# Performance work log

Measured on AMD Instinct MI355X. Metric: run time of the kernel, lower is better.

The kernel has to match this reference:

```python
import jax, jax.numpy as jnp
import numpy as np

SCALE = 100.0

def square_distance(src, dst):
    # src: [B,N,D], dst: [B,M,D] -> [B,N,M] squared euclidean distances
    d = -2.0 * jnp.einsum('bnd,bmd->bnm', src, dst)
    d = d + jnp.sum(src * src, axis=-1)[:, :, None]
    d = d + jnp.sum(dst * dst, axis=-1)[:, None, :]
    return d

def setup_inputs() -> dict:
    key = jax.random.key(0)
    k1, k2 = jax.random.split(key)
    B, N, M, D = 8, 8192, 8192, 3
    pred = jax.random.normal(k1, (B, N, D), dtype=jnp.float32)
    gt = jax.random.normal(k2, (B, M, D), dtype=jnp.float32)
    return {"pred": pred, "gt": gt}

def reference(pred, gt):
    dis = square_distance(pred, gt)              # [B,N,M]
    pred_to_gt = jnp.min(dis, axis=2).mean(axis=1)  # [B]
    gt_to_pred = jnp.min(dis, axis=1).mean(axis=1)  # [B]
    return (0.5 * pred_to_gt + 0.5 * gt_to_pred).mean() * SCALE
```

## Files before the change

kernel.cpp:

```cpp
#include <hip/hip_runtime.h>


#define B_DIM 8
#define N_DIM 8192
#define MT    (N_DIM / 32)
#define CH    16
#define NC    (MT / CH)
#define BLOCK 256
#define PPW   2

typedef short  bf16x8 __attribute__((ext_vector_type(8)));
typedef float  f32x16 __attribute__((ext_vector_type(16)));

__device__ __forceinline__ unsigned short bf16_rne(float f) {
    unsigned int u = __float_as_uint(f);
    u += 0x7fffu + ((u >> 16) & 1u);
    return (unsigned short)(u >> 16);
}
__device__ __forceinline__ float bf16f(unsigned short h) {
    return __uint_as_float(((unsigned int)h) << 16);
}

__global__ __launch_bounds__(256) void chamfer_prep(
    const float* __restrict__ pred, const float* __restrict__ gt,
    unsigned short* __restrict__ bpack, float* __restrict__ out)
{
    const int i   = blockIdx.x * 256 + threadIdx.x;
    if (i == 0) out[0] = 0.0f;
    const int dir = i >> 16;
    const int bm  = i & 0xFFFF;
    const float* dst = dir ? pred : gt;
    const float x = dst[3*bm+0], y = dst[3*bm+1], z = dst[3*bm+2];
    const unsigned short hx = bf16_rne(x), hy = bf16_rne(y), hz = bf16_rne(z);
    const unsigned short lx = bf16_rne(x - bf16f(hx));
    const unsigned short ly = bf16_rne(y - bf16f(hy));
    const unsigned short lz = bf16_rne(z - bf16f(hz));
    const float gn = x*x + y*y + z*z;
    const unsigned short gnh = bf16_rne(gn), gnl = bf16_rne(gn - bf16f(gnh));
    const unsigned short one = 0x3F80;

    const int b  = bm >> 13, m = bm & (N_DIM - 1);
    const int mt = m >> 5,   c = m & 31;
    const int dirb = (dir << 3) | b;
    unsigned short* p0 = bpack + ((size_t)(dirb * MT + mt) * 64 + c) * 8;
    unsigned short* p1 = p0 + 32 * 8;
    bf16x8 h0 = {(short)hx,(short)hy,(short)hz,(short)lx,(short)ly,(short)lz,(short)hx,(short)hy};
    bf16x8 h1 = {(short)hz,(short)one,(short)one,(short)gnh,(short)gnl,0,0,0};
    *(bf16x8*)p0 = h0;
    *(bf16x8*)p1 = h1;
}

__global__ __launch_bounds__(BLOCK, 2) void chamfer_partial(
    const float* __restrict__ pred, const float* __restrict__ gt,
    const bf16x8* __restrict__ bpack, float* __restrict__ out)
{
    __shared__ bf16x8 sbuf[2][CH * 64];
    __shared__ float wsum[4];
    const int dirb = blockIdx.x;
    const int dir  = dirb >> 3, b = dirb & 7;
    const int w    = threadIdx.x >> 6, lane = threadIdx.x & 63;
    const int half = lane >> 5,  col = lane & 31;

    const float* src  = dir ? gt : pred;
    const float* srcb = src + (size_t)b * N_DIM * 3;

    bf16x8 afrag[PPW];
    #pragma unroll
    for (int p = 0; p < PPW; ++p) {
        const int ntile = (blockIdx.y * 4 + w) * PPW + p;
        const int n = ntile * 32 + col;
        const float x = srcb[3*n+0], y = srcb[3*n+1], z = srcb[3*n+2];
        const float ax = -2.f*x, ay = -2.f*y, az = -2.f*z;
        const unsigned short ahx = bf16_rne(ax), ahy = bf16_rne(ay), ahz = bf16_rne(az);
        const unsigned short alx = bf16_rne(ax - bf16f(ahx));
        const unsigned short aly = bf16_rne(ay - bf16f(ahy));
        const unsigned short alz = bf16_rne(az - bf16f(ahz));
        const float pn = x*x + y*y + z*z;
        const unsigned short pnh = bf16_rne(pn), pnl = bf16_rne(pn - bf16f(pnh));
        const unsigned short one = 0x3F80;
        bf16x8 a0 = {(short)ahx,(short)ahy,(short)ahz,(short)ahx,(short)ahy,(short)ahz,(short)alx,(short)aly};
        bf16x8 a1 = {(short)alz,(short)pnh,(short)pnl,(short)one,(short)one,0,0,0};
        afrag[p] = (half == 0) ? a0 : a1;
    }

    const bf16x8* bp = bpack + (size_t)dirb * MT * 64;
    const f32x16 czero = {0.f,0.f,0.f,0.f,0.f,0.f,0.f,0.f,
                          0.f,0.f,0.f,0.f,0.f,0.f,0.f,0.f};
    float best[PPW][16];
    #pragma unroll
    for (int p = 0; p < PPW; ++p)
        #pragma unroll
        for (int r = 0; r < 16; ++r) best[p][r] = 1e30f;

    bf16x8 rg[4];
    const int soff = w * 256 + lane;
    #define GLOAD(c) { const bf16x8* g = bp + (size_t)(c) * (CH*64) + soff; \
        _Pragma("unroll") for (int i = 0; i < 4; ++i) rg[i] = g[i * 64]; }
    #define SWRITE(pb) { bf16x8* s = &sbuf[pb][soff]; \
        _Pragma("unroll") for (int i = 0; i < 4; ++i) s[i * 64] = rg[i]; }

    GLOAD(0); SWRITE(0); GLOAD(1);
    __syncthreads();

    for (int c = 0; c < NC; ++c) {
        const int pb = c & 1;
        if (c + 1 < NC) SWRITE(pb ^ 1);
        if (c + 2 < NC) GLOAD(c + 2);
        #pragma unroll 8
        for (int j = 0; j < CH; ++j) {
            const bf16x8 bc = sbuf[pb][j * 64 + lane];
            #pragma unroll
            for (int p = 0; p < PPW; ++p) {
                f32x16 d = __builtin_amdgcn_mfma_f32_32x32x16_bf16(afrag[p], bc, czero, 0, 0, 0);
                #pragma unroll
                for (int r = 0; r < 16; ++r) best[p][r] = fminf(best[p][r], d[r]);
            }
        }
        __syncthreads();
    }

    float bsum = 0.f;
    #pragma unroll
    for (int p = 0; p < PPW; ++p) {
        float s = 0.f;
        #pragma unroll
        for (int r = 0; r < 16; ++r) {
            float v = best[p][r];
            v = fminf(v, __shfl_xor(v, 1,  64));
            v = fminf(v, __shfl_xor(v, 2,  64));
            v = fminf(v, __shfl_xor(v, 4,  64));
            v = fminf(v, __shfl_xor(v, 8,  64));
            v = fminf(v, __shfl_xor(v, 16, 64));
            s += v;
        }
        bsum += s + __shfl_xor(s, 32, 64);
    }
    if (lane == 0) wsum[w] = bsum;
    __syncthreads();
    if (threadIdx.x == 0) {
        const float scale = 100.0f * 0.5f / ((float)B_DIM * (float)N_DIM);
        atomicAdd(out, (wsum[0] + wsum[1] + wsum[2] + wsum[3]) * scale);
    }
}

extern "C" void kernel_launch(void* const* d_in, const int* in_sizes, int n_in,
                              void* d_out, int out_size, void* d_ws, size_t ws_size,
                              hipStream_t stream) {
    const float* pred = (const float*)d_in[0];
    const float* gt   = (const float*)d_in[1];
    float* out = (float*)d_out;
    unsigned short* bpack = (unsigned short*)d_ws;

    chamfer_prep<<<(2 * B_DIM * N_DIM) / 256, 256, 0, stream>>>(pred, gt, bpack, out);

    dim3 grid(16, N_DIM / (32 * 4 * PPW));
    chamfer_partial<<<grid, BLOCK, 0, stream>>>(pred, gt, (const bf16x8*)bpack, out);
}
```

Before: 95.53 us.

## Split M across wave pairs, use direct global-to-LDS loads, raise occupancy

Each block now covers 128 query points instead of 256. The four waves form two pairs over N-tiles, and the waves in a pair take separate halves of the M range. The partial row minima from those halves are combined through LDS at the end. Global data is staged straight into LDS with global_load_lds instead of going through registers, and the launch bound allows 4 blocks per CU. The aim is more blocks in flight and more overlap of loads with MFMA work. The cost is a second LDS reduction step, and the synchronisation of the async LDS loads may be fragile.

```diff
diff --git a/kernel.cpp b/kernel.cpp
--- a/kernel.cpp
+++ b/kernel.cpp
@@ -4,8 +4,8 @@
 #define B_DIM 8
 #define N_DIM 8192
 #define MT    (N_DIM / 32)
-#define CH    16
-#define NC    (MT / CH)
+#define CH    8
+#define NC    16
 #define BLOCK 256
 #define PPW   2
 
@@ -50,16 +50,18 @@
     *(bf16x8*)p1 = h1;
 }
 
-__global__ __launch_bounds__(BLOCK, 2) void chamfer_partial(
+__global__ __launch_bounds__(BLOCK, 4) void chamfer_partial(
     const float* __restrict__ pred, const float* __restrict__ gt,
     const bf16x8* __restrict__ bpack, float* __restrict__ out)
 {
-    __shared__ bf16x8 sbuf[2][CH * 64];
-    __shared__ float wsum[4];
+    __shared__ bf16x8 sbuf[2][1024];
+    __shared__ float wsum[2];
     const int dirb = blockIdx.x;
     const int dir  = dirb >> 3, b = dirb & 7;
     const int w    = threadIdx.x >> 6, lane = threadIdx.x & 63;
-    const int half = lane >> 5,  col = lane & 31;
+    const int halfk = lane >> 5,  col = lane & 31;
+    const int nsub = w & 1;
+    const int mh   = w >> 1;
 
     const float* src  = dir ? gt : pred;
     const float* srcb = src + (size_t)b * N_DIM * 3;
@@ -67,7 +69,7 @@
     bf16x8 afrag[PPW];
     #pragma unroll
     for (int p = 0; p < PPW; ++p) {
-        const int ntile = (blockIdx.y * 4 + w) * PPW + p;
+        const int ntile = blockIdx.y * 4 + nsub * 2 + p;
         const int n = ntile * 32 + col;
         const float x = srcb[3*n+0], y = srcb[3*n+1], z = srcb[3*n+2];
         const float ax = -2.f*x, ay = -2.f*y, az = -2.f*z;
@@ -80,10 +82,16 @@
         const unsigned short one = 0x3F80;
         bf16x8 a0 = {(short)ahx,(short)ahy,(short)ahz,(short)ahx,(short)ahy,(short)ahz,(short)alx,(short)aly};
         bf16x8 a1 = {(short)alz,(short)pnh,(short)pnl,(short)one,(short)one,0,0,0};
-        afrag[p] = (half == 0) ? a0 : a1;
+        afrag[p] = (halfk == 0) ? a0 : a1;
     }
 
-    const bf16x8* bp = bpack + (size_t)dirb * MT * 64;
+    const bf16x8* bp = bpack + (size_t)dirb * (MT * 64);
+
+#define STAGE(pb_, c_) { _Pragma("unroll") for (int i = 0; i < 4; ++i) { \
+        const bf16x8* g_ = bp + ((i >> 1) * 8192 + (c_) * 512 + (i & 1) * 256 + w * 64 + lane); \
+        __builtin_amdgcn_global_load_lds((__attribute__((address_space(1))) void*)g_, \
+            (__attribute__((address_space(3))) void*)&sbuf[pb_][i * 256 + w * 64], 16, 0, 0); } }
+
     const f32x16 czero = {0.f,0.f,0.f,0.f,0.f,0.f,0.f,0.f,
                           0.f,0.f,0.f,0.f,0.f,0.f,0.f,0.f};
     float best[PPW][16];
@@ -92,54 +100,61 @@
         #pragma unroll
         for (int r = 0; r < 16; ++r) best[p][r] = 1e30f;
 
-    bf16x8 rg[4];
-    const int soff = w * 256 + lane;
-    #define GLOAD(c) { const bf16x8* g = bp + (size_t)(c) * (CH*64) + soff; \
-        _Pragma("unroll") for (int i = 0; i < 4; ++i) rg[i] = g[i * 64]; }
-    #define SWRITE(pb) { bf16x8* s = &sbuf[pb][soff]; \
-        _Pragma("unroll") for (int i = 0; i < 4; ++i) s[i * 64] = rg[i]; }
-
-    GLOAD(0); SWRITE(0); GLOAD(1);
+    STAGE(0, 0);
     __syncthreads();
 
     for (int c = 0; c < NC; ++c) {
         const int pb = c & 1;
-        if (c + 1 < NC) SWRITE(pb ^ 1);
-        if (c + 2 < NC) GLOAD(c + 2);
-        #pragma unroll 8
-        for (int j = 0; j < CH; ++j) {
-            const bf16x8 bc = sbuf[pb][j * 64 + lane];
+        if (c + 1 < NC) STAGE(pb ^ 1, c + 1);
+        const bf16x8* sb = &sbuf[pb][mh * 512];
+        #pragma unroll
+        for (int j = 0; j < CH; j += 2) {
+            const bf16x8 bc0 = sb[j * 64 + lane];
+            const bf16x8 bc1 = sb[(j + 1) * 64 + lane];
             #pragma unroll
             for (int p = 0; p < PPW; ++p) {
-                f32x16 d = __builtin_amdgcn_mfma_f32_32x32x16_bf16(afrag[p], bc, czero, 0, 0, 0);
+                const f32x16 d0 = __builtin_amdgcn_mfma_f32_32x32x16_bf16(afrag[p], bc0, czero, 0, 0, 0);
+                const f32x16 d1 = __builtin_amdgcn_mfma_f32_32x32x16_bf16(afrag[p], bc1, czero, 0, 0, 0);
                 #pragma unroll
-                for (int r = 0; r < 16; ++r) best[p][r] = fminf(best[p][r], d[r]);
+                for (int r = 0; r < 16; ++r)
+                    best[p][r] = fminf(fminf(best[p][r], d0[r]), d1[r]);
             }
         }
         __syncthreads();
     }
 
-    float bsum = 0.f;
-    #pragma unroll
-    for (int p = 0; p < PPW; ++p) {
-        float s = 0.f;
+    float* cbuf = (float*)&sbuf[0][0];
+    if (mh == 1) {
         #pragma unroll
-        for (int r = 0; r < 16; ++r) {
-            float v = best[p][r];
-            v = fminf(v, __shfl_xor(v, 1,  64));
-            v = fminf(v, __shfl_xor(v, 2,  64));
-            v = fminf(v, __shfl_xor(v, 4,  64));
-            v = fminf(v, __shfl_xor(v, 8,  64));
-            v = fminf(v, __shfl_xor(v, 16, 64));
-            s += v;
+        for (int p = 0; p < PPW; ++p)
+            #pragma unroll
+            for (int r = 0; r < 16; ++r)
+                cbuf[(p * 16 + r) * 128 + nsub * 64 + lane] = best[p][r];
+    }
+    __syncthreads();
+    if (mh == 0) {
+        float bsum = 0.f;
+        #pragma unroll
+        for (int p = 0; p < PPW; ++p) {
+            float s = 0.f;
+            #pragma unroll
+            for (int r = 0; r < 16; ++r) {
+                float v = fminf(best[p][r], cbuf[(p * 16 + r) * 128 + nsub * 64 + lane]);
+                v = fminf(v, __shfl_xor(v, 1,  64));
+                v = fminf(v, __shfl_xor(v, 2,  64));
+                v = fminf(v, __shfl_xor(v, 4,  64));
+                v = fminf(v, __shfl_xor(v, 8,  64));
+                v = fminf(v, __shfl_xor(v, 16, 64));
+                s += v;
+            }
+            bsum += s + __shfl_xor(s, 32, 64);
         }
-        bsum += s + __shfl_xor(s, 32, 64);
+        if (lane == 0) wsum[nsub] = bsum;
     }
-    if (lane == 0) wsum[w] = bsum;
     __syncthreads();
     if (threadIdx.x == 0) {
         const float scale = 100.0f * 0.5f / ((float)B_DIM * (float)N_DIM);
-        atomicAdd(out, (wsum[0] + wsum[1] + wsum[2] + wsum[3]) * scale);
+        atomicAdd(out, (wsum[0] + wsum[1]) * scale);
     }
 }
 
@@ -153,6 +168,6 @@
 
     chamfer_prep<<<(2 * B_DIM * N_DIM) / 256, 256, 0, stream>>>(pred, gt, bpack, out);
 
-    dim3 grid(16, N_DIM / (32 * 4 * PPW));
+    dim3 grid(16, N_DIM / 128);
     chamfer_partial<<<grid, BLOCK, 0, stream>>>(pred, gt, (const bf16x8*)bpack, out);
 }
```

Measured after the change: 116.8 us. 22.2% more time.

## Stream B fragments from global into registers with inline-asm MFMA and min3 pipeline

Applied to the files above, without the earlier changes.

Drops the LDS double-buffered staging of the packed B tiles. Each wave now loads B fragments straight from global memory into registers, issued one batch ahead. MFMAs are hand-scheduled in inline asm, four per batch, and alternate between two accumulator sets so the v_min3 reductions of one batch overlap the MFMAs of the next. The final atomicAdd is replaced by per-block partial sums written to workspace plus a small third reduction kernel. This removes LDS traffic and barriers, but it depends on L2/cache hits for the repeated global loads, on manual hazard s_nops, and it adds a kernel launch.

```diff
diff --git a/kernel.cpp b/kernel.cpp
--- a/kernel.cpp
+++ b/kernel.cpp
@@ -4,10 +4,9 @@
 #define B_DIM 8
 #define N_DIM 8192
 #define MT    (N_DIM / 32)
-#define CH    16
-#define NC    (MT / CH)
 #define BLOCK 256
 #define PPW   2
+#define NBLK  512
 
 typedef short  bf16x8 __attribute__((ext_vector_type(8)));
 typedef float  f32x16 __attribute__((ext_vector_type(16)));
@@ -52,14 +51,13 @@
 
 __global__ __launch_bounds__(BLOCK, 2) void chamfer_partial(
     const float* __restrict__ pred, const float* __restrict__ gt,
-    const bf16x8* __restrict__ bpack, float* __restrict__ out)
+    const bf16x8* __restrict__ bpack, float* __restrict__ part)
 {
-    __shared__ bf16x8 sbuf[2][CH * 64];
     __shared__ float wsum[4];
     const int dirb = blockIdx.x;
     const int dir  = dirb >> 3, b = dirb & 7;
     const int w    = threadIdx.x >> 6, lane = threadIdx.x & 63;
-    const int half = lane >> 5,  col = lane & 31;
+    const int halfk = lane >> 5,  col = lane & 31;
 
     const float* src  = dir ? gt : pred;
     const float* srcb = src + (size_t)b * N_DIM * 3;
@@ -67,7 +65,7 @@
     bf16x8 afrag[PPW];
     #pragma unroll
     for (int p = 0; p < PPW; ++p) {
-        const int ntile = (blockIdx.y * 4 + w) * PPW + p;
+        const int ntile = blockIdx.y * 8 + w * 2 + p;
         const int n = ntile * 32 + col;
         const float x = srcb[3*n+0], y = srcb[3*n+1], z = srcb[3*n+2];
         const float ax = -2.f*x, ay = -2.f*y, az = -2.f*z;
@@ -80,44 +78,59 @@
         const unsigned short one = 0x3F80;
         bf16x8 a0 = {(short)ahx,(short)ahy,(short)ahz,(short)ahx,(short)ahy,(short)ahz,(short)alx,(short)aly};
         bf16x8 a1 = {(short)alz,(short)pnh,(short)pnl,(short)one,(short)one,0,0,0};
-        afrag[p] = (half == 0) ? a0 : a1;
+        afrag[p] = (halfk == 0) ? a0 : a1;
     }
 
-    const bf16x8* bp = bpack + (size_t)dirb * MT * 64;
-    const f32x16 czero = {0.f,0.f,0.f,0.f,0.f,0.f,0.f,0.f,
-                          0.f,0.f,0.f,0.f,0.f,0.f,0.f,0.f};
     float best[PPW][16];
     #pragma unroll
     for (int p = 0; p < PPW; ++p)
         #pragma unroll
         for (int r = 0; r < 16; ++r) best[p][r] = 1e30f;
 
-    bf16x8 rg[4];
-    const int soff = w * 256 + lane;
-    #define GLOAD(c) { const bf16x8* g = bp + (size_t)(c) * (CH*64) + soff; \
-        _Pragma("unroll") for (int i = 0; i < 4; ++i) rg[i] = g[i * 64]; }
-    #define SWRITE(pb) { bf16x8* s = &sbuf[pb][soff]; \
-        _Pragma("unroll") for (int i = 0; i < 4; ++i) s[i * 64] = rg[i]; }
+    const bf16x8* bq = bpack + (size_t)dirb * (MT * 64) + lane;
 
-    GLOAD(0); SWRITE(0); GLOAD(1);
-    __syncthreads();
+#define BATCH(q0_, q1_, q2_, q3_, c0_, c1_) \
+        asm volatile( \
+            "v_mfma_f32_32x32x16_bf16 %0, %4, %6, 0\n\t" \
+            "v_mfma_f32_32x32x16_bf16 %1, %4, %7, 0\n\t" \
+            "v_mfma_f32_32x32x16_bf16 %2, %5, %6, 0\n\t" \
+            "v_mfma_f32_32x32x16_bf16 %3, %5, %7, 0" \
+            : "=&v"(q0_), "=&v"(q1_), "=&v"(q2_), "=&v"(q3_) \
+            : "v"(afrag[0]), "v"(afrag[1]), "v"(c0_), "v"(c1_));
 
-    for (int c = 0; c < NC; ++c) {
-        const int pb = c & 1;
-        if (c + 1 < NC) SWRITE(pb ^ 1);
-        if (c + 2 < NC) GLOAD(c + 2);
-        #pragma unroll 8
-        for (int j = 0; j < CH; ++j) {
-            const bf16x8 bc = sbuf[pb][j * 64 + lane];
-            #pragma unroll
-            for (int p = 0; p < PPW; ++p) {
-                f32x16 d = __builtin_amdgcn_mfma_f32_32x32x16_bf16(afrag[p], bc, czero, 0, 0, 0);
-                #pragma unroll
-                for (int r = 0; r < 16; ++r) best[p][r] = fminf(best[p][r], d[r]);
-            }
-        }
-        __syncthreads();
+#define MIN3Q(q0_, q1_, q2_, q3_) { \
+        _Pragma("unroll") \
+        for (int r = 0; r < 16; ++r) \
+            asm volatile("v_min3_f32 %0, %0, %1, %2" \
+                : "+v"(best[0][r]) : "v"((q0_)[r]), "v"((q1_)[r])); \
+        _Pragma("unroll") \
+        for (int r = 0; r < 16; ++r) \
+            asm volatile("v_min3_f32 %0, %0, %1, %2" \
+                : "+v"(best[1][r]) : "v"((q2_)[r]), "v"((q3_)[r])); \
     }
+
+    f32x16 dE0, dE1, dE2, dE3;
+    f32x16 dO0, dO1, dO2, dO3;
+
+    bf16x8 cA0 = bq[0],   cA1 = bq[64];
+    bf16x8 cB0 = bq[128], cB1 = bq[192];
+    BATCH(dE0, dE1, dE2, dE3, cA0, cA1);
+    cA0 = bq[256]; cA1 = bq[320];
+
+    for (int t = 0; t < 63; ++t) {
+        BATCH(dO0, dO1, dO2, dO3, cB0, cB1);
+        { const bf16x8* nx = bq + ((2*t + 3) & 127) * 128;
+          cB0 = nx[0]; cB1 = nx[64]; }
+        MIN3Q(dE0, dE1, dE2, dE3);
+        BATCH(dE0, dE1, dE2, dE3, cA0, cA1);
+        { const bf16x8* nx = bq + ((2*t + 4) & 127) * 128;
+          cA0 = nx[0]; cA1 = nx[64]; }
+        MIN3Q(dO0, dO1, dO2, dO3);
+    }
+    BATCH(dO0, dO1, dO2, dO3, cB0, cB1);
+    MIN3Q(dE0, dE1, dE2, dE3);
+    asm volatile("s_nop 7\n\ts_nop 7\n\ts_nop 7\n\ts_nop 3");
+    MIN3Q(dO0, dO1, dO2, dO3);
 
     float bsum = 0.f;
     #pragma unroll
@@ -137,9 +150,28 @@
     }
     if (lane == 0) wsum[w] = bsum;
     __syncthreads();
+    if (threadIdx.x == 0)
+        part[blockIdx.y * 16 + blockIdx.x] =
+            wsum[0] + wsum[1] + wsum[2] + wsum[3];
+}
+
+__global__ __launch_bounds__(256) void chamfer_final(
+    const float* __restrict__ part, float* __restrict__ out)
+{
+    float s = part[threadIdx.x] + part[256 + threadIdx.x];
+    s += __shfl_xor(s, 1,  64);
+    s += __shfl_xor(s, 2,  64);
+    s += __shfl_xor(s, 4,  64);
+    s += __shfl_xor(s, 8,  64);
+    s += __shfl_xor(s, 16, 64);
+    s += __shfl_xor(s, 32, 64);
+    __shared__ float ws4[4];
+    const int w = threadIdx.x >> 6, lane = threadIdx.x & 63;
+    if (lane == 0) ws4[w] = s;
+    __syncthreads();
     if (threadIdx.x == 0) {
         const float scale = 100.0f * 0.5f / ((float)B_DIM * (float)N_DIM);
-        atomicAdd(out, (wsum[0] + wsum[1] + wsum[2] + wsum[3]) * scale);
+        out[0] = (ws4[0] + ws4[1] + ws4[2] + ws4[3]) * scale;
     }
 }
 
@@ -150,9 +182,12 @@
     const float* gt   = (const float*)d_in[1];
     float* out = (float*)d_out;
     unsigned short* bpack = (unsigned short*)d_ws;
+    float* part = (float*)((char*)d_ws + ((size_t)4 << 20));
 
     chamfer_prep<<<(2 * B_DIM * N_DIM) / 256, 256, 0, stream>>>(pred, gt, bpack, out);
 
-    dim3 grid(16, N_DIM / (32 * 4 * PPW));
-    chamfer_partial<<<grid, BLOCK, 0, stream>>>(pred, gt, (const bf16x8*)bpack, out);
+    dim3 grid(16, N_DIM / 256);
+    chamfer_partial<<<grid, BLOCK, 0, stream>>>(pred, gt, (const bf16x8*)bpack, part);
+
+    chamfer_final<<<1, 256, 0, stream>>>(part, out);
 }
```

New measurement: 94.13 us. About the same (-1.5%).
